# Kernel optimization log

Hardware: AMD Instinct MI355X
Metric: run time of the kernel (lower is better)

## Reference

```python
import jax, jax.numpy as jnp
import numpy as np

B, N, H = 8, 256, 768
P = 128          # path_hidden_size
HEADS = 12
D = H // HEADS   # 64
EPS = 1e-5


def layer_norm(x, g, b):
    mu = jnp.mean(x, axis=-1, keepdims=True)
    var = jnp.mean((x - mu) ** 2, axis=-1, keepdims=True)
    return (x - mu) * jax.lax.rsqrt(var + EPS) * g + b


def setup_inputs() -> dict:
    key = jax.random.key(0)
    ks = jax.random.split(key, 16)
    s = 0.02
    return {
        "nodes": jax.random.normal(ks[0], (B, N, H), jnp.float32),
        "bias": jax.random.normal(ks[1], (B, HEADS, N, N), jnp.float32),
        "paths": jax.random.normal(ks[2], (B, N, N, P), jnp.float32),
        "Wq": jax.random.normal(ks[3], (H, H), jnp.float32) * s,
        "bq": jnp.zeros((H,), jnp.float32),
        "Wk": jax.random.normal(ks[4], (H, H), jnp.float32) * s,
        "bk": jnp.zeros((H,), jnp.float32),
        "Wv": jax.random.normal(ks[5], (H, H), jnp.float32) * s,
        "bv": jnp.zeros((H,), jnp.float32),
        "Wsk": jax.random.normal(ks[6], (P, D), jnp.float32) * s,
        "bsk": jnp.zeros((D,), jnp.float32),
        "Wsv": jax.random.normal(ks[7], (P, D), jnp.float32) * s,
        "bsv": jnp.zeros((D,), jnp.float32),
        "Wo": jax.random.normal(ks[8], (H, H), jnp.float32) * s,
        "bo": jnp.zeros((H,), jnp.float32),
        "g_path": jnp.ones((P,), jnp.float32),
        "b_path": jnp.zeros((P,), jnp.float32),
        "g_out": jnp.ones((H,), jnp.float32),
        "b_out": jnp.zeros((H,), jnp.float32),
    }


def reference(nodes, bias, paths, Wq, bq, Wk, bk, Wv, bv, Wsk, bsk, Wsv, bsv,
              Wo, bo, g_path, b_path, g_out, b_out):
    # q/k/v: [B,N,H] -> [B,heads,N,D]
    def split(x):
        return x.reshape(B, N, HEADS, D).transpose(0, 2, 1, 3)

    q = split(nodes @ Wq + bq)
    k = split(nodes @ Wk + bk)
    v = split(nodes @ Wv + bv)

    pn = layer_norm(paths, g_path, b_path)          # [B,N,N,P]
    struct_k = pn @ Wsk + bsk                       # [B,N,N,D]
    struct_v = pn @ Wsv + bsv                       # [B,N,N,D]

    q = q * (D ** -0.5)
    # content scores + per-query-row structural scores + bias
    w = (jnp.einsum('bhqd,bhkd->bhqk', q, k)
         + jnp.einsum('bhqd,bqkd->bhqk', q, struct_k)
         + bias)
    w = jax.nn.softmax(w, axis=-1)                  # [B,heads,N,N]

    out = (jnp.einsum('bhqk,bhkd->bhqd', w, v)
           + jnp.einsum('bhqk,bqkd->bhqd', w, struct_v))
    out = out.transpose(0, 2, 1, 3).reshape(B, N, H)  # combine heads
    out = jax.nn.relu(out @ Wo + bo)
    # dropout is identity in eval mode
    return layer_norm(nodes + out, g_out, b_out)
```

## Files before the change

### kernel.cpp

```cpp
#include <hip/hip_runtime.h>
#include <stdint.h>

#define Bb 8
#define Nn 256
#define Hh 768
#define Pp 128
#define HEADS 12
#define Dd 64
#define EPSf 1e-5f

typedef __attribute__((ext_vector_type(8))) short bhalf8;
typedef __attribute__((ext_vector_type(4))) float f32x4;

__device__ __forceinline__ unsigned short f2bf(float f) {
    union { float f; unsigned u; } v; v.f = f;
    unsigned r = v.u + 0x7FFFu + ((v.u >> 16) & 1u);
    return (unsigned short)(r >> 16);
}

__global__ __launch_bounds__(256) void k_transpose4(const float* __restrict__ a0, const float* __restrict__ a1,
                                                    const float* __restrict__ a2, const float* __restrict__ a3,
                                                    unsigned short* __restrict__ o0, unsigned short* __restrict__ o1,
                                                    unsigned short* __restrict__ o2, unsigned short* __restrict__ o3) {
    __shared__ float tile[32][33];
    int z = blockIdx.z;
    const float* in = (z == 0) ? a0 : (z == 1) ? a1 : (z == 2) ? a2 : a3;
    unsigned short* out = (z == 0) ? o0 : (z == 1) ? o1 : (z == 2) ? o2 : o3;
    const int R = 768, C = 768;
    int c0 = blockIdx.x * 32, r0 = blockIdx.y * 32;
    int tx = threadIdx.x & 31, ty = threadIdx.x >> 5;
    for (int i = ty; i < 32; i += 8)
        tile[i][tx] = in[(size_t)(r0 + i) * C + c0 + tx];
    __syncthreads();
    for (int i = ty; i < 32; i += 8)
        out[(size_t)(c0 + i) * R + r0 + tx] = f2bf(tile[tx][i]);
}

__global__ __launch_bounds__(256) void k_transpose_small(const float* __restrict__ a0, const float* __restrict__ a1,
                                                         unsigned short* __restrict__ o0, unsigned short* __restrict__ o1) {
    __shared__ float tile[32][33];
    int z = blockIdx.z;
    const float* in = (z == 0) ? a0 : a1;
    unsigned short* out = (z == 0) ? o0 : o1;
    const int R = 128, C = 64;
    int c0 = blockIdx.x * 32, r0 = blockIdx.y * 32;
    int tx = threadIdx.x & 31, ty = threadIdx.x >> 5;
    for (int i = ty; i < 32; i += 8)
        tile[i][tx] = in[(size_t)(r0 + i) * C + c0 + tx];
    __syncthreads();
    for (int i = ty; i < 32; i += 8)
        out[(size_t)(c0 + i) * R + r0 + tx] = f2bf(tile[tx][i]);
}

__global__ __launch_bounds__(256) void k_qkv(const float* __restrict__ nodes,
                                             const unsigned short* __restrict__ Wt,
                                             const float* __restrict__ bq, const float* __restrict__ bk,
                                             const float* __restrict__ bv,
                                             float* __restrict__ qs, float* __restrict__ kk,
                                             float* __restrict__ vv) {
    __shared__ __align__(16) unsigned short Alds[64 * 72];
    __shared__ __align__(16) unsigned short Blds[128 * 72];
    int tid = threadIdx.x;
    int m0 = blockIdx.y * 64;
    int n0 = blockIdx.x * 128;
    int w = tid >> 6, lane = tid & 63;
    int wm = w >> 1, wn = w & 1;
    int lm = lane & 15, lq = lane >> 4;
    f32x4 acc[2][4];
#pragma unroll
    for (int i = 0; i < 2; i++)
#pragma unroll
        for (int j = 0; j < 4; j++) acc[i][j] = (f32x4){0.f, 0.f, 0.f, 0.f};

    for (int kt = 0; kt < 768; kt += 64) {
#pragma unroll
        for (int t = 0; t < 4; t++) {
            int c = t * 256 + tid;
            int row = c >> 4, cc = c & 15;
            float4 v = *(const float4*)(nodes + (size_t)(m0 + row) * 768 + kt + cc * 4);
            uint2 uu;
            uu.x = (unsigned)f2bf(v.x) | ((unsigned)f2bf(v.y) << 16);
            uu.y = (unsigned)f2bf(v.z) | ((unsigned)f2bf(v.w) << 16);
            *(uint2*)(Alds + row * 72 + cc * 4) = uu;
        }
#pragma unroll
        for (int t = 0; t < 4; t++) {
            int c = t * 256 + tid;
            int n = c >> 3, kc = c & 7;
            uint4 v = *(const uint4*)(Wt + (size_t)(n0 + n) * 768 + kt + kc * 8);
            *(uint4*)(Blds + n * 72 + kc * 8) = v;
        }
        __syncthreads();
#pragma unroll
        for (int ks = 0; ks < 2; ks++) {
            bhalf8 af[2];
#pragma unroll
            for (int mi = 0; mi < 2; mi++)
                af[mi] = *(const bhalf8*)(Alds + (wm * 32 + mi * 16 + lm) * 72 + ks * 32 + lq * 8);
#pragma unroll
            for (int nt = 0; nt < 4; nt++) {
                bhalf8 bf = *(const bhalf8*)(Blds + (wn * 64 + nt * 16 + lm) * 72 + ks * 32 + lq * 8);
#pragma unroll
                for (int mi = 0; mi < 2; mi++)
                    acc[mi][nt] = __builtin_amdgcn_mfma_f32_16x16x32_bf16(af[mi], bf, acc[mi][nt], 0, 0, 0);
            }
        }
        __syncthreads();
    }
    int wsel = n0 / 768;
    int nb = n0 % 768;
    const float* bias = (wsel == 0) ? bq : (wsel == 1) ? bk : bv;
    float* dst = (wsel == 0) ? qs : (wsel == 1) ? kk : vv;
    float scale = (wsel == 0) ? 0.125f : 1.0f;
#pragma unroll
    for (int mi = 0; mi < 2; mi++)
#pragma unroll
        for (int nt = 0; nt < 4; nt++)
#pragma unroll
            for (int r = 0; r < 4; r++) {
                int row = m0 + wm * 32 + mi * 16 + lq * 4 + r;
                int col = nb + wn * 64 + nt * 16 + lm;
                int hh = col >> 6, d = col & 63;
                int b = row >> 8, qn = row & 255;
                float val = (acc[mi][nt][r] + bias[col]) * scale;
                dst[(((size_t)b * HEADS + hh) * Nn + qn) * Dd + d] = val;
            }
}

__global__ __launch_bounds__(256) void k_scores(const float* __restrict__ qs,
                                                const float* __restrict__ kk,
                                                const float* __restrict__ bias,
                                                float* __restrict__ wg) {
    __shared__ __align__(16) unsigned short Alds[64 * 72];
    __shared__ __align__(16) unsigned short Blds[64 * 72];
    int tid = threadIdx.x;
    int bh = blockIdx.z;
    int m0 = blockIdx.y * 64;
    int n0 = blockIdx.x * 64;
    int w = tid >> 6, lane = tid & 63, lm = lane & 15, lq = lane >> 4;
    const float* Abase = qs + ((size_t)bh * Nn + m0) * Dd;
    const float* Bbase = kk + ((size_t)bh * Nn + n0) * Dd;
#pragma unroll
    for (int t = 0; t < 4; t++) {
        int c = t * 256 + tid;
        int row = c >> 4, cc = c & 15;
        float4 va = *(const float4*)(Abase + (size_t)row * 64 + cc * 4);
        uint2 ua;
        ua.x = (unsigned)f2bf(va.x) | ((unsigned)f2bf(va.y) << 16);
        ua.y = (unsigned)f2bf(va.z) | ((unsigned)f2bf(va.w) << 16);
        *(uint2*)(Alds + row * 72 + cc * 4) = ua;
        float4 vb = *(const float4*)(Bbase + (size_t)row * 64 + cc * 4);
        uint2 ub;
        ub.x = (unsigned)f2bf(vb.x) | ((unsigned)f2bf(vb.y) << 16);
        ub.y = (unsigned)f2bf(vb.z) | ((unsigned)f2bf(vb.w) << 16);
        *(uint2*)(Blds + row * 72 + cc * 4) = ub;
    }
    __syncthreads();
    f32x4 acc[4];
#pragma unroll
    for (int i = 0; i < 4; i++) acc[i] = (f32x4){0.f, 0.f, 0.f, 0.f};
#pragma unroll
    for (int ks = 0; ks < 2; ks++) {
        bhalf8 af = *(const bhalf8*)(Alds + (w * 16 + lm) * 72 + ks * 32 + lq * 8);
#pragma unroll
        for (int nt = 0; nt < 4; nt++) {
            bhalf8 bf = *(const bhalf8*)(Blds + (nt * 16 + lm) * 72 + ks * 32 + lq * 8);
            acc[nt] = __builtin_amdgcn_mfma_f32_16x16x32_bf16(af, bf, acc[nt], 0, 0, 0);
        }
    }
#pragma unroll
    for (int nt = 0; nt < 4; nt++)
#pragma unroll
        for (int r = 0; r < 4; r++) {
            int row = m0 + w * 16 + lq * 4 + r;
            int col = n0 + nt * 16 + lm;
            size_t idx = ((size_t)bh * Nn + row) * Nn + col;
            wg[idx] = acc[nt][r] + bias[idx];
        }
}

__global__ __launch_bounds__(256) void k_structproj(const float* __restrict__ paths,
                                                    const unsigned short* __restrict__ Wskvt,
                                                    const float* __restrict__ gp, const float* __restrict__ bp,
                                                    const float* __restrict__ bsk, const float* __restrict__ bsv,
                                                    unsigned short* __restrict__ skv) {
    __shared__ __align__(16) unsigned short pn[64 * 136];
    __shared__ __align__(16) unsigned short Bt[128 * 136];
    int tid = threadIdx.x;
    size_t r0 = (size_t)blockIdx.x * 64;
    int w = tid >> 6, lane = tid & 63, lm = lane & 15, lq = lane >> 4;
#pragma unroll
    for (int t = 0; t < 8; t++) {
        int c = t * 256 + tid;
        int n = c >> 4, kc = c & 15;
        uint4 v = *(const uint4*)(Wskvt + n * 128 + kc * 8);
        *(uint4*)(Bt + n * 136 + kc * 8) = v;
    }
    float4 g0 = *(const float4*)(gp + lm * 4);
    float4 g1 = *(const float4*)(gp + 64 + lm * 4);
    float4 bb0 = *(const float4*)(bp + lm * 4);
    float4 bb1 = *(const float4*)(bp + 64 + lm * 4);
#pragma unroll
    for (int it = 0; it < 4; it++) {
        int row_l = w * 16 + it * 4 + lq;
        size_t row = r0 + row_l;
        const float* pr = paths + row * 128;
        float4 x0 = *(const float4*)(pr + lm * 4);
        float4 x1 = *(const float4*)(pr + 64 + lm * 4);
        float s = (x0.x + x0.y) + (x0.z + x0.w) + (x1.x + x1.y) + (x1.z + x1.w);
        float s2 = x0.x * x0.x + x0.y * x0.y + x0.z * x0.z + x0.w * x0.w
                 + x1.x * x1.x + x1.y * x1.y + x1.z * x1.z + x1.w * x1.w;
#pragma unroll
        for (int mk = 1; mk < 16; mk <<= 1) {
            s += __shfl_xor(s, mk);
            s2 += __shfl_xor(s2, mk);
        }
        float mu = s * (1.f / 128.f);
        float var = s2 * (1.f / 128.f) - mu * mu;
        float rs = rsqrtf(var + EPSf);
        float p0 = (x0.x - mu) * rs * g0.x + bb0.x;
        float p1 = (x0.y - mu) * rs * g0.y + bb0.y;
        float p2 = (x0.z - mu) * rs * g0.z + bb0.z;
        float p3 = (x0.w - mu) * rs * g0.w + bb0.w;
        float p4 = (x1.x - mu) * rs * g1.x + bb1.x;
        float p5 = (x1.y - mu) * rs * g1.y + bb1.y;
        float p6 = (x1.z - mu) * rs * g1.z + bb1.z;
        float p7 = (x1.w - mu) * rs * g1.w + bb1.w;
        uint2 ua, ub;
        ua.x = (unsigned)f2bf(p0) | ((unsigned)f2bf(p1) << 16);
        ua.y = (unsigned)f2bf(p2) | ((unsigned)f2bf(p3) << 16);
        ub.x = (unsigned)f2bf(p4) | ((unsigned)f2bf(p5) << 16);
        ub.y = (unsigned)f2bf(p6) | ((unsigned)f2bf(p7) << 16);
        *(uint2*)(pn + row_l * 136 + lm * 4) = ua;
        *(uint2*)(pn + row_l * 136 + 64 + lm * 4) = ub;
    }
    __syncthreads();
    f32x4 acc[8];
#pragma unroll
    for (int i = 0; i < 8; i++) acc[i] = (f32x4){0.f, 0.f, 0.f, 0.f};
#pragma unroll
    for (int ks = 0; ks < 4; ks++) {
        bhalf8 af = *(const bhalf8*)(pn + (w * 16 + lm) * 136 + ks * 32 + lq * 8);
#pragma unroll
        for (int nt = 0; nt < 8; nt++) {
            bhalf8 bf = *(const bhalf8*)(Bt + (nt * 16 + lm) * 136 + ks * 32 + lq * 8);
            acc[nt] = __builtin_amdgcn_mfma_f32_16x16x32_bf16(af, bf, acc[nt], 0, 0, 0);
        }
    }
    __syncthreads();
#pragma unroll
    for (int nt = 0; nt < 8; nt++) {
        int col = nt * 16 + lm;
        float bias = (col < 64) ? bsk[col] : bsv[col - 64];
#pragma unroll
        for (int r = 0; r < 4; r++) {
            int row_l = w * 16 + lq * 4 + r;
            pn[row_l * 136 + col] = f2bf(acc[nt][r] + bias);
        }
    }
    __syncthreads();
#pragma unroll
    for (int i = 0; i < 4; i++) {
        int c = i * 256 + tid;
        int row = c >> 4, chunk = c & 15;
        uint4 v = *(const uint4*)(pn + row * 136 + chunk * 8);
        *(uint4*)(skv + (r0 + row) * 128 + chunk * 8) = v;
    }
}

__global__ __launch_bounds__(256) void k_attn(const float* __restrict__ qs,
                                              const unsigned short* __restrict__ skv,
                                              float* __restrict__ wg,
                                              float* __restrict__ attn) {
    __shared__ __align__(16) unsigned short SKV[256 * 72];
    __shared__ __align__(16) unsigned short A2[16 * 264];
    __shared__ __align__(16) unsigned short Ql[16 * 72];
    __shared__ float redm[16][4];
    __shared__ float reds[16][4];
    int tid = threadIdx.x;
    int bq = blockIdx.x;
    int b = bq >> 8, q = bq & 255;
    int w = tid >> 6, lane = tid & 63, lm = lane & 15, lq = lane >> 4;
    if (tid < 192) {
        int h = tid >> 4, dc = (tid & 15) * 4;
        float4 v = *(const float4*)(qs + (((size_t)b * HEADS + h) * Nn + q) * Dd + dc);
        uint2 u;
        u.x = (unsigned)f2bf(v.x) | ((unsigned)f2bf(v.y) << 16);
        u.y = (unsigned)f2bf(v.z) | ((unsigned)f2bf(v.w) << 16);
        *(uint2*)(Ql + h * 72 + dc) = u;
    } else {
        int t = tid - 192;
        int h = 12 + (t >> 4), dc = (t & 15) * 4;
        uint2 z; z.x = 0; z.y = 0;
        *(uint2*)(Ql + h * 72 + dc) = z;
    }
    const unsigned short* rowb = skv + (size_t)bq * 256 * 128;
#pragma unroll
    for (int i = 0; i < 8; i++) {
        int c = i * 256 + tid;
        int k = c >> 3, j = c & 7;
        uint4 v = *(const uint4*)(rowb + (size_t)k * 128 + j * 8);
        *(uint4*)(SKV + k * 72 + j * 8) = v;
    }
    __syncthreads();
    f32x4 acc1[4];
#pragma unroll
    for (int i = 0; i < 4; i++) acc1[i] = (f32x4){0.f, 0.f, 0.f, 0.f};
#pragma unroll
    for (int ks = 0; ks < 2; ks++) {
        bhalf8 af = *(const bhalf8*)(Ql + lm * 72 + ks * 32 + lq * 8);
#pragma unroll
        for (int nt = 0; nt < 4; nt++) {
            int n0 = (w * 4 + nt) * 16;
            bhalf8 bf = *(const bhalf8*)(SKV + (n0 + lm) * 72 + ks * 32 + lq * 8);
            acc1[nt] = __builtin_amdgcn_mfma_f32_16x16x32_bf16(af, bf, acc1[nt], 0, 0, 0);
        }
    }
    size_t wbase = ((size_t)b * HEADS) * Nn * Nn + (size_t)q * Nn;
    float S[4][4];
#pragma unroll
    for (int nt = 0; nt < 4; nt++)
#pragma unroll
        for (int r = 0; r < 4; r++) {
            int row = lq * 4 + r;
            int col = (w * 4 + nt) * 16 + lm;
            float wgv = (row < 12) ? wg[wbase + (size_t)row * (Nn * Nn) + col] : 0.f;
            S[nt][r] = acc1[nt][r] + wgv;
        }
    float m4[4];
#pragma unroll
    for (int r = 0; r < 4; r++)
        m4[r] = fmaxf(fmaxf(S[0][r], S[1][r]), fmaxf(S[2][r], S[3][r]));
#pragma unroll
    for (int mk = 1; mk < 16; mk <<= 1)
#pragma unroll
        for (int r = 0; r < 4; r++) m4[r] = fmaxf(m4[r], __shfl_xor(m4[r], mk));
    if (lm == 0) {
#pragma unroll
        for (int r = 0; r < 4; r++) redm[lq * 4 + r][w] = m4[r];
    }
    __syncthreads();
    float rowmax[4];
#pragma unroll
    for (int r = 0; r < 4; r++) {
        int row = lq * 4 + r;
        rowmax[r] = fmaxf(fmaxf(redm[row][0], redm[row][1]), fmaxf(redm[row][2], redm[row][3]));
    }
    float P[4][4], psum[4];
#pragma unroll
    for (int r = 0; r < 4; r++) {
#pragma unroll
        for (int nt = 0; nt < 4; nt++) P[nt][r] = __expf(S[nt][r] - rowmax[r]);
        psum[r] = (P[0][r] + P[1][r]) + (P[2][r] + P[3][r]);
    }
#pragma unroll
    for (int mk = 1; mk < 16; mk <<= 1)
#pragma unroll
        for (int r = 0; r < 4; r++) psum[r] += __shfl_xor(psum[r], mk);
    if (lm == 0) {
#pragma unroll
        for (int r = 0; r < 4; r++) reds[lq * 4 + r][w] = psum[r];
    }
    __syncthreads();
    float inv[4];
#pragma unroll
    for (int r = 0; r < 4; r++) {
        int row = lq * 4 + r;
        inv[r] = 1.f / (((reds[row][0] + reds[row][1]) + (reds[row][2] + reds[row][3])));
    }
#pragma unroll
    for (int nt = 0; nt < 4; nt++)
#pragma unroll
        for (int r = 0; r < 4; r++) {
            int row = lq * 4 + r;
            int col = (w * 4 + nt) * 16 + lm;
            float p = P[nt][r] * inv[r];
            A2[row * 264 + col] = f2bf(p);
            if (row < 12) wg[wbase + (size_t)row * (Nn * Nn) + col] = p;
        }
#pragma unroll
    for (int i = 0; i < 8; i++) {
        int c = i * 256 + tid;
        int k = c >> 3, j = c & 7;
        uint4 v = *(const uint4*)(rowb + (size_t)k * 128 + 64 + j * 8);
        *(uint4*)(SKV + k * 72 + j * 8) = v;
    }
    __syncthreads();
    f32x4 acc2 = (f32x4){0.f, 0.f, 0.f, 0.f};
#pragma unroll
    for (int ks = 0; ks < 8; ks++) {
        bhalf8 af = *(const bhalf8*)(A2 + lm * 264 + ks * 32 + lq * 8);
        bhalf8 bf;
#pragma unroll
        for (int j = 0; j < 8; j++)
            bf[j] = (short)SKV[(ks * 32 + lq * 8 + j) * 72 + w * 16 + lm];
        acc2 = __builtin_amdgcn_mfma_f32_16x16x32_bf16(af, bf, acc2, 0, 0, 0);
    }
#pragma unroll
    for (int r = 0; r < 4; r++) {
        int row = lq * 4 + r;
        if (row < 12) attn[(size_t)bq * Hh + row * 64 + w * 16 + lm] = acc2[r];
    }
}

__global__ __launch_bounds__(256) void k_ctxout(const float* __restrict__ wg,
                                                const float* __restrict__ vv,
                                                float* __restrict__ attn) {
    __shared__ __align__(16) float Al[64 * 68];
    __shared__ __align__(16) float Bl[64 * 68];
    int tid = threadIdx.x;
    int bh = blockIdx.y;
    int m0 = blockIdx.x * 64;
    int b = bh / 12, h = bh % 12;
    int tx = tid & 15, ty = tid >> 4;
    int c0 = tx * 4, r0 = ty * 4;
    float acc[4][4];
#pragma unroll
    for (int i = 0; i < 4; i++)
#pragma unroll
        for (int j = 0; j < 4; j++) acc[i][j] = 0.f;
    const float* Abase = wg + ((size_t)bh * Nn + m0) * Nn;
    const float* Bbase = vv + (size_t)bh * Nn * Dd;
    for (int kt = 0; kt < 256; kt += 64) {
#pragma unroll
        for (int t = 0; t < 4; t++) {
            int c = t * 256 + tid;
            int row = c >> 4, cc = c & 15;
            *(float4*)(Al + row * 68 + cc * 4) = *(const float4*)(Abase + (size_t)row * 256 + kt + cc * 4);
            *(float4*)(Bl + row * 68 + cc * 4) = *(const float4*)(Bbase + (size_t)(kt + row) * 64 + cc * 4);
        }
        __syncthreads();
#pragma unroll 8
        for (int k = 0; k < 64; k++) {
            float4 bv4 = *(const float4*)(Bl + k * 68 + c0);
            float a0 = Al[(r0 + 0) * 68 + k];
            float a1 = Al[(r0 + 1) * 68 + k];
            float a2 = Al[(r0 + 2) * 68 + k];
            float a3 = Al[(r0 + 3) * 68 + k];
            acc[0][0] += a0 * bv4.x; acc[0][1] += a0 * bv4.y; acc[0][2] += a0 * bv4.z; acc[0][3] += a0 * bv4.w;
            acc[1][0] += a1 * bv4.x; acc[1][1] += a1 * bv4.y; acc[1][2] += a1 * bv4.z; acc[1][3] += a1 * bv4.w;
            acc[2][0] += a2 * bv4.x; acc[2][1] += a2 * bv4.y; acc[2][2] += a2 * bv4.z; acc[2][3] += a2 * bv4.w;
            acc[3][0] += a3 * bv4.x; acc[3][1] += a3 * bv4.y; acc[3][2] += a3 * bv4.z; acc[3][3] += a3 * bv4.w;
        }
        __syncthreads();
    }
#pragma unroll
    for (int i = 0; i < 4; i++)
#pragma unroll
        for (int j = 0; j < 4; j++) {
            size_t o = ((size_t)b * Nn + m0 + r0 + i) * Hh + h * 64 + c0 + j;
            attn[o] += acc[i][j];
        }
}

__global__ __launch_bounds__(256) void k_outproj(const float* __restrict__ attn,
                                                 const unsigned short* __restrict__ Wot,
                                                 const float* __restrict__ bo,
                                                 const float* __restrict__ nodes,
                                                 float* __restrict__ tmp) {
    __shared__ __align__(16) unsigned short Alds[64 * 72];
    __shared__ __align__(16) unsigned short Blds[128 * 72];
    int tid = threadIdx.x;
    int m0 = blockIdx.y * 64;
    int n0 = blockIdx.x * 128;
    int w = tid >> 6, lane = tid & 63;
    int wm = w >> 1, wn = w & 1;
    int lm = lane & 15, lq = lane >> 4;
    f32x4 acc[2][4];
#pragma unroll
    for (int i = 0; i < 2; i++)
#pragma unroll
        for (int j = 0; j < 4; j++) acc[i][j] = (f32x4){0.f, 0.f, 0.f, 0.f};
    for (int kt = 0; kt < 768; kt += 64) {
#pragma unroll
        for (int t = 0; t < 4; t++) {
            int c = t * 256 + tid;
            int row = c >> 4, cc = c & 15;
            float4 v = *(const float4*)(attn + (size_t)(m0 + row) * 768 + kt + cc * 4);
            uint2 uu;
            uu.x = (unsigned)f2bf(v.x) | ((unsigned)f2bf(v.y) << 16);
            uu.y = (unsigned)f2bf(v.z) | ((unsigned)f2bf(v.w) << 16);
            *(uint2*)(Alds + row * 72 + cc * 4) = uu;
        }
#pragma unroll
        for (int t = 0; t < 4; t++) {
            int c = t * 256 + tid;
            int n = c >> 3, kc = c & 7;
            uint4 v = *(const uint4*)(Wot + (size_t)(n0 + n) * 768 + kt + kc * 8);
            *(uint4*)(Blds + n * 72 + kc * 8) = v;
        }
        __syncthreads();
#pragma unroll
        for (int ks = 0; ks < 2; ks++) {
            bhalf8 af[2];
#pragma unroll
            for (int mi = 0; mi < 2; mi++)
                af[mi] = *(const bhalf8*)(Alds + (wm * 32 + mi * 16 + lm) * 72 + ks * 32 + lq * 8);
#pragma unroll
            for (int nt = 0; nt < 4; nt++) {
                bhalf8 bf = *(const bhalf8*)(Blds + (wn * 64 + nt * 16 + lm) * 72 + ks * 32 + lq * 8);
#pragma unroll
                for (int mi = 0; mi < 2; mi++)
                    acc[mi][nt] = __builtin_amdgcn_mfma_f32_16x16x32_bf16(af[mi], bf, acc[mi][nt], 0, 0, 0);
            }
        }
        __syncthreads();
    }
#pragma unroll
    for (int mi = 0; mi < 2; mi++)
#pragma unroll
        for (int nt = 0; nt < 4; nt++)
#pragma unroll
            for (int r = 0; r < 4; r++) {
                int row = m0 + wm * 32 + mi * 16 + lq * 4 + r;
                int col = n0 + wn * 64 + nt * 16 + lm;
                float val = acc[mi][nt][r] + bo[col];
                val = fmaxf(val, 0.f) + nodes[(size_t)row * 768 + col];
                tmp[(size_t)row * 768 + col] = val;
            }
}

__global__ __launch_bounds__(256) void k_finalln(const float* __restrict__ tmp,
                                                 const float* __restrict__ go,
                                                 const float* __restrict__ bout,
                                                 float* __restrict__ out) {
    __shared__ float rs1[4], rs2[4];
    int m = blockIdx.x, tid = threadIdx.x;
    int lane = tid & 63, wid = tid >> 6;
    const float* row = tmp + (size_t)m * 768;
    float x0 = row[tid], x1 = row[tid + 256], x2 = row[tid + 512];
    float s = x0 + x1 + x2;
    float s2 = x0 * x0 + x1 * x1 + x2 * x2;
#pragma unroll
    for (int mk = 32; mk; mk >>= 1) {
        s += __shfl_xor(s, mk);
        s2 += __shfl_xor(s2, mk);
    }
    if (lane == 0) { rs1[wid] = s; rs2[wid] = s2; }
    __syncthreads();
    s = rs1[0] + rs1[1] + rs1[2] + rs1[3];
    s2 = rs2[0] + rs2[1] + rs2[2] + rs2[3];
    float mu = s * (1.f / 768.f);
    float var = s2 * (1.f / 768.f) - mu * mu;
    float rstd = rsqrtf(var + EPSf);
    float* orow = out + (size_t)m * 768;
    orow[tid] = (x0 - mu) * rstd * go[tid] + bout[tid];
    orow[tid + 256] = (x1 - mu) * rstd * go[tid + 256] + bout[tid + 256];
    orow[tid + 512] = (x2 - mu) * rstd * go[tid + 512] + bout[tid + 512];
}

extern "C" void kernel_launch(void* const* d_in, const int* in_sizes, int n_in,
                              void* d_out, int out_size, void* d_ws, size_t ws_size,
                              hipStream_t stream) {
    const float* nodes = (const float*)d_in[0];
    const float* bias  = (const float*)d_in[1];
    const float* paths = (const float*)d_in[2];
    const float* Wq = (const float*)d_in[3];  const float* bq  = (const float*)d_in[4];
    const float* Wk = (const float*)d_in[5];  const float* bk  = (const float*)d_in[6];
    const float* Wv = (const float*)d_in[7];  const float* bv  = (const float*)d_in[8];
    const float* Wsk = (const float*)d_in[9]; const float* bsk = (const float*)d_in[10];
    const float* Wsv = (const float*)d_in[11];const float* bsv = (const float*)d_in[12];
    const float* Wo = (const float*)d_in[13]; const float* bo  = (const float*)d_in[14];
    const float* gp = (const float*)d_in[15]; const float* bp  = (const float*)d_in[16];
    const float* go = (const float*)d_in[17]; const float* bout= (const float*)d_in[18];
    float* out = (float*)d_out;

    char* ws = (char*)d_ws;
    size_t off = 0;
    auto carve = [&](size_t bytes) -> char* {
        char* p = ws + off;
        off += (bytes + 255) & ~(size_t)255;
        return p;
    };
    float* qs   = (float*)carve((size_t)Bb * HEADS * Nn * Dd * 4);
    float* kk   = (float*)carve((size_t)Bb * HEADS * Nn * Dd * 4);
    float* vv   = (float*)carve((size_t)Bb * HEADS * Nn * Dd * 4);
    float* wg   = (float*)carve((size_t)Bb * HEADS * Nn * Nn * 4);
    float* attn = (float*)carve((size_t)Bb * Nn * Hh * 4);
    float* tmp  = (float*)carve((size_t)Bb * Nn * Hh * 4);
    unsigned short* Wqkvt = (unsigned short*)carve((size_t)3 * 768 * 768 * 2);
    unsigned short* Wot   = (unsigned short*)carve((size_t)768 * 768 * 2);
    unsigned short* Wskvt = (unsigned short*)carve((size_t)128 * 128 * 2);
    unsigned short* skv   = (unsigned short*)carve((size_t)Bb * Nn * Nn * 128 * 2);
    (void)ws_size; (void)in_sizes; (void)n_in; (void)out_size;

    hipLaunchKernelGGL(k_transpose4, dim3(24, 24, 4), dim3(256), 0, stream,
                       Wq, Wk, Wv, Wo,
                       Wqkvt, Wqkvt + (size_t)768 * 768, Wqkvt + (size_t)2 * 768 * 768, Wot);
    hipLaunchKernelGGL(k_transpose_small, dim3(2, 4, 2), dim3(256), 0, stream,
                       Wsk, Wsv, Wskvt, Wskvt + (size_t)64 * 128);

    hipLaunchKernelGGL(k_qkv, dim3(18, 32), dim3(256), 0, stream, nodes, Wqkvt, bq, bk, bv, qs, kk, vv);
    hipLaunchKernelGGL(k_scores, dim3(4, 4, 96), dim3(256), 0, stream, qs, kk, bias, wg);
    hipLaunchKernelGGL(k_structproj, dim3(8192), dim3(256), 0, stream, paths, Wskvt, gp, bp, bsk, bsv, skv);
    hipLaunchKernelGGL(k_attn, dim3(2048), dim3(256), 0, stream, qs, skv, wg, attn);
    hipLaunchKernelGGL(k_ctxout, dim3(4, 96), dim3(256), 0, stream, wg, vv, attn);
    hipLaunchKernelGGL(k_outproj, dim3(6, 32), dim3(256), 0, stream, attn, Wot, bo, nodes, tmp);
    hipLaunchKernelGGL(k_finalln, dim3(2048), dim3(256), 0, stream, tmp, go, bout, out);
}
```

Baseline: 559.5 us.

## Fuse path layernorm and struct projection into attention kernel, fold LN affine into weights

Removes the separate k_structproj kernel and its 268MB bf16 skv intermediate: each attention block now reads its row of paths, layer-normalizes in registers and projects through MFMA directly, keeping struct_k/struct_v in LDS. The LN gain is folded into the transposed weights and the LN bias into a precomputed projection bias. struct_v is stored transposed in LDS so the PV MFMA uses vector loads instead of scalar gathers. In exchange each block does more register-heavy work, with a launch bound asking for two blocks per CU.

```diff
diff --git a/kernel.cpp b/kernel.cpp
--- a/kernel.cpp
+++ b/kernel.cpp
@@ -37,6 +37,7 @@
 }
 
 __global__ __launch_bounds__(256) void k_transpose_small(const float* __restrict__ a0, const float* __restrict__ a1,
+                                                         const float* __restrict__ gp,
                                                          unsigned short* __restrict__ o0, unsigned short* __restrict__ o1) {
     __shared__ float tile[32][33];
     int z = blockIdx.z;
@@ -48,8 +49,21 @@
     for (int i = ty; i < 32; i += 8)
         tile[i][tx] = in[(size_t)(r0 + i) * C + c0 + tx];
     __syncthreads();
+    float g = gp[r0 + tx];
     for (int i = ty; i < 32; i += 8)
-        out[(size_t)(c0 + i) * R + r0 + tx] = f2bf(tile[tx][i]);
+        out[(size_t)(c0 + i) * R + r0 + tx] = f2bf(tile[tx][i] * g);
+}
+
+__global__ __launch_bounds__(128) void k_prep_bias(const float* __restrict__ Wsk, const float* __restrict__ Wsv,
+                                                   const float* __restrict__ bp,
+                                                   const float* __restrict__ bsk, const float* __restrict__ bsv,
+                                                   float* __restrict__ bskv2) {
+    int d = threadIdx.x;
+    const float* W = (d < 64) ? Wsk : Wsv;
+    int dd = d & 63;
+    float s = (d < 64) ? bsk[dd] : bsv[dd];
+    for (int p2 = 0; p2 < 128; p2++) s += bp[p2] * W[p2 * 64 + dd];
+    bskv2[d] = s;
 }
 
 __global__ __launch_bounds__(256) void k_qkv(const float* __restrict__ nodes,
@@ -179,154 +193,157 @@
         }
 }
 
-__global__ __launch_bounds__(256) void k_structproj(const float* __restrict__ paths,
-                                                    const unsigned short* __restrict__ Wskvt,
-                                                    const float* __restrict__ gp, const float* __restrict__ bp,
-                                                    const float* __restrict__ bsk, const float* __restrict__ bsv,
-                                                    unsigned short* __restrict__ skv) {
-    __shared__ __align__(16) unsigned short pn[64 * 136];
-    __shared__ __align__(16) unsigned short Bt[128 * 136];
-    int tid = threadIdx.x;
-    size_t r0 = (size_t)blockIdx.x * 64;
-    int w = tid >> 6, lane = tid & 63, lm = lane & 15, lq = lane >> 4;
-#pragma unroll
-    for (int t = 0; t < 8; t++) {
-        int c = t * 256 + tid;
-        int n = c >> 4, kc = c & 15;
-        uint4 v = *(const uint4*)(Wskvt + n * 128 + kc * 8);
-        *(uint4*)(Bt + n * 136 + kc * 8) = v;
-    }
-    float4 g0 = *(const float4*)(gp + lm * 4);
-    float4 g1 = *(const float4*)(gp + 64 + lm * 4);
-    float4 bb0 = *(const float4*)(bp + lm * 4);
-    float4 bb1 = *(const float4*)(bp + 64 + lm * 4);
-#pragma unroll
-    for (int it = 0; it < 4; it++) {
-        int row_l = w * 16 + it * 4 + lq;
-        size_t row = r0 + row_l;
-        const float* pr = paths + row * 128;
-        float4 x0 = *(const float4*)(pr + lm * 4);
-        float4 x1 = *(const float4*)(pr + 64 + lm * 4);
-        float s = (x0.x + x0.y) + (x0.z + x0.w) + (x1.x + x1.y) + (x1.z + x1.w);
-        float s2 = x0.x * x0.x + x0.y * x0.y + x0.z * x0.z + x0.w * x0.w
-                 + x1.x * x1.x + x1.y * x1.y + x1.z * x1.z + x1.w * x1.w;
-#pragma unroll
-        for (int mk = 1; mk < 16; mk <<= 1) {
-            s += __shfl_xor(s, mk);
-            s2 += __shfl_xor(s2, mk);
-        }
-        float mu = s * (1.f / 128.f);
-        float var = s2 * (1.f / 128.f) - mu * mu;
-        float rs = rsqrtf(var + EPSf);
-        float p0 = (x0.x - mu) * rs * g0.x + bb0.x;
-        float p1 = (x0.y - mu) * rs * g0.y + bb0.y;
-        float p2 = (x0.z - mu) * rs * g0.z + bb0.z;
-        float p3 = (x0.w - mu) * rs * g0.w + bb0.w;
-        float p4 = (x1.x - mu) * rs * g1.x + bb1.x;
-        float p5 = (x1.y - mu) * rs * g1.y + bb1.y;
-        float p6 = (x1.z - mu) * rs * g1.z + bb1.z;
-        float p7 = (x1.w - mu) * rs * g1.w + bb1.w;
-        uint2 ua, ub;
-        ua.x = (unsigned)f2bf(p0) | ((unsigned)f2bf(p1) << 16);
-        ua.y = (unsigned)f2bf(p2) | ((unsigned)f2bf(p3) << 16);
-        ub.x = (unsigned)f2bf(p4) | ((unsigned)f2bf(p5) << 16);
-        ub.y = (unsigned)f2bf(p6) | ((unsigned)f2bf(p7) << 16);
-        *(uint2*)(pn + row_l * 136 + lm * 4) = ua;
-        *(uint2*)(pn + row_l * 136 + 64 + lm * 4) = ub;
-    }
-    __syncthreads();
-    f32x4 acc[8];
-#pragma unroll
-    for (int i = 0; i < 8; i++) acc[i] = (f32x4){0.f, 0.f, 0.f, 0.f};
-#pragma unroll
-    for (int ks = 0; ks < 4; ks++) {
-        bhalf8 af = *(const bhalf8*)(pn + (w * 16 + lm) * 136 + ks * 32 + lq * 8);
-#pragma unroll
-        for (int nt = 0; nt < 8; nt++) {
-            bhalf8 bf = *(const bhalf8*)(Bt + (nt * 16 + lm) * 136 + ks * 32 + lq * 8);
-            acc[nt] = __builtin_amdgcn_mfma_f32_16x16x32_bf16(af, bf, acc[nt], 0, 0, 0);
-        }
-    }
-    __syncthreads();
-#pragma unroll
-    for (int nt = 0; nt < 8; nt++) {
-        int col = nt * 16 + lm;
-        float bias = (col < 64) ? bsk[col] : bsv[col - 64];
-#pragma unroll
-        for (int r = 0; r < 4; r++) {
-            int row_l = w * 16 + lq * 4 + r;
-            pn[row_l * 136 + col] = f2bf(acc[nt][r] + bias);
-        }
-    }
-    __syncthreads();
-#pragma unroll
-    for (int i = 0; i < 4; i++) {
-        int c = i * 256 + tid;
-        int row = c >> 4, chunk = c & 15;
-        uint4 v = *(const uint4*)(pn + row * 136 + chunk * 8);
-        *(uint4*)(skv + (r0 + row) * 128 + chunk * 8) = v;
-    }
-}
-
-__global__ __launch_bounds__(256) void k_attn(const float* __restrict__ qs,
-                                              const unsigned short* __restrict__ skv,
-                                              float* __restrict__ wg,
-                                              float* __restrict__ attn) {
-    __shared__ __align__(16) unsigned short SKV[256 * 72];
+__global__ __launch_bounds__(256, 2) void k_attn(const float* __restrict__ qs,
+                                                 const float* __restrict__ paths,
+                                                 const unsigned short* __restrict__ Wskvt,
+                                                 const float* __restrict__ bskv2,
+                                                 float* __restrict__ wg,
+                                                 float* __restrict__ attn) {
+    __shared__ __align__(16) unsigned short SKbuf[256 * 72];
     __shared__ __align__(16) unsigned short A2[16 * 264];
-    __shared__ __align__(16) unsigned short Ql[16 * 72];
-    __shared__ float redm[16][4];
-    __shared__ float reds[16][4];
+    __shared__ float redm[64];
+    __shared__ float reds[64];
+    unsigned short* SVT = SKbuf;
+
     int tid = threadIdx.x;
     int bq = blockIdx.x;
     int b = bq >> 8, q = bq & 255;
     int w = tid >> 6, lane = tid & 63, lm = lane & 15, lq = lane >> 4;
-    if (tid < 192) {
-        int h = tid >> 4, dc = (tid & 15) * 4;
-        float4 v = *(const float4*)(qs + (((size_t)b * HEADS + h) * Nn + q) * Dd + dc);
-        uint2 u;
-        u.x = (unsigned)f2bf(v.x) | ((unsigned)f2bf(v.y) << 16);
-        u.y = (unsigned)f2bf(v.z) | ((unsigned)f2bf(v.w) << 16);
-        *(uint2*)(Ql + h * 72 + dc) = u;
-    } else {
-        int t = tid - 192;
-        int h = 12 + (t >> 4), dc = (t & 15) * 4;
-        uint2 z; z.x = 0; z.y = 0;
-        *(uint2*)(Ql + h * 72 + dc) = z;
-    }
-    const unsigned short* rowb = skv + (size_t)bq * 256 * 128;
-#pragma unroll
-    for (int i = 0; i < 8; i++) {
-        int c = i * 256 + tid;
-        int k = c >> 3, j = c & 7;
-        uint4 v = *(const uint4*)(rowb + (size_t)k * 128 + j * 8);
-        *(uint4*)(SKV + k * 72 + j * 8) = v;
-    }
-    __syncthreads();
-    f32x4 acc1[4];
-#pragma unroll
-    for (int i = 0; i < 4; i++) acc1[i] = (f32x4){0.f, 0.f, 0.f, 0.f};
-#pragma unroll
-    for (int ks = 0; ks < 2; ks++) {
-        bhalf8 af = *(const bhalf8*)(Ql + lm * 72 + ks * 32 + lq * 8);
-#pragma unroll
-        for (int nt = 0; nt < 4; nt++) {
-            int n0 = (w * 4 + nt) * 16;
-            bhalf8 bf = *(const bhalf8*)(SKV + (n0 + lm) * 72 + ks * 32 + lq * 8);
-            acc1[nt] = __builtin_amdgcn_mfma_f32_16x16x32_bf16(af, bf, acc1[nt], 0, 0, 0);
-        }
-    }
-    size_t wbase = ((size_t)b * HEADS) * Nn * Nn + (size_t)q * Nn;
-    float S[4][4];
-#pragma unroll
-    for (int nt = 0; nt < 4; nt++)
+
+    bhalf8 af1[2];
+    {
+        bhalf8 z = (bhalf8){0, 0, 0, 0, 0, 0, 0, 0};
+        af1[0] = z; af1[1] = z;
+        if (lm < 12) {
+            const float* qp = qs + (((size_t)b * HEADS + lm) * Nn + q) * Dd;
+#pragma unroll
+            for (int ks = 0; ks < 2; ks++) {
+                float4 v0 = *(const float4*)(qp + ks * 32 + lq * 8);
+                float4 v1 = *(const float4*)(qp + ks * 32 + lq * 8 + 4);
+                bhalf8 t;
+                t[0] = (short)f2bf(v0.x); t[1] = (short)f2bf(v0.y);
+                t[2] = (short)f2bf(v0.z); t[3] = (short)f2bf(v0.w);
+                t[4] = (short)f2bf(v1.x); t[5] = (short)f2bf(v1.y);
+                t[6] = (short)f2bf(v1.z); t[7] = (short)f2bf(v1.w);
+                af1[ks] = t;
+            }
+        }
+    }
+    float bv_[8];
+#pragma unroll
+    for (int nt = 0; nt < 8; nt++) bv_[nt] = bskv2[nt * 16 + lm];
+
+    const float* ppath = paths + (size_t)bq * (256 * 128);
+    f32x4 accSV[2][2][4];
+
+#pragma unroll
+    for (int p = 0; p < 2; p++) {
+        f32x4 acc[2][8];
+#pragma unroll
+        for (int i = 0; i < 2; i++)
+#pragma unroll
+            for (int j = 0; j < 8; j++) acc[i][j] = (f32x4){0.f, 0.f, 0.f, 0.f};
+        bhalf8 afr[2][4];
+#pragma unroll
+        for (int mi = 0; mi < 2; mi++) {
+            int R = w * 64 + p * 32 + mi * 16 + lm;
+            const float* pr = ppath + (size_t)R * 128;
+            float x[32];
+#pragma unroll
+            for (int ks = 0; ks < 4; ks++) {
+                float4 a = *(const float4*)(pr + ks * 32 + lq * 8);
+                float4 c = *(const float4*)(pr + ks * 32 + lq * 8 + 4);
+                x[ks * 8 + 0] = a.x; x[ks * 8 + 1] = a.y; x[ks * 8 + 2] = a.z; x[ks * 8 + 3] = a.w;
+                x[ks * 8 + 4] = c.x; x[ks * 8 + 5] = c.y; x[ks * 8 + 6] = c.z; x[ks * 8 + 7] = c.w;
+            }
+            float s = 0.f, s2 = 0.f;
+#pragma unroll
+            for (int i = 0; i < 32; i++) { s += x[i]; s2 += x[i] * x[i]; }
+            s  += __shfl_xor(s, 16);  s2 += __shfl_xor(s2, 16);
+            s  += __shfl_xor(s, 32);  s2 += __shfl_xor(s2, 32);
+            float mu = s * (1.f / 128.f);
+            float var = s2 * (1.f / 128.f) - mu * mu;
+            float rs = rsqrtf(var + EPSf);
+#pragma unroll
+            for (int ks = 0; ks < 4; ks++) {
+                bhalf8 t;
+#pragma unroll
+                for (int j = 0; j < 8; j++)
+                    t[j] = (short)f2bf((x[ks * 8 + j] - mu) * rs);
+                afr[mi][ks] = t;
+            }
+        }
+#pragma unroll
+        for (int ks = 0; ks < 4; ks++) {
+#pragma unroll
+            for (int nt = 0; nt < 8; nt++) {
+                bhalf8 bf = *(const bhalf8*)(Wskvt + (size_t)(nt * 16 + lm) * 128 + ks * 32 + lq * 8);
+#pragma unroll
+                for (int mi = 0; mi < 2; mi++)
+                    acc[mi][nt] = __builtin_amdgcn_mfma_f32_16x16x32_bf16(afr[mi][ks], bf, acc[mi][nt], 0, 0, 0);
+            }
+        }
+#pragma unroll
+        for (int mi = 0; mi < 2; mi++) {
+#pragma unroll
+            for (int nt = 0; nt < 4; nt++) {
+                int col = nt * 16 + lm;
+#pragma unroll
+                for (int rr = 0; rr < 4; rr++) {
+                    int R2 = w * 64 + p * 32 + mi * 16 + lq * 4 + rr;
+                    SKbuf[R2 * 72 + col] = f2bf(acc[mi][nt][rr] + bv_[nt]);
+                }
+            }
+#pragma unroll
+            for (int nt = 0; nt < 4; nt++) accSV[p][mi][nt] = acc[mi][nt + 4];
+        }
+    }
+    __syncthreads();
+
+    size_t wbase = ((size_t)b * HEADS) * (Nn * Nn) + (size_t)q * Nn;
+    float wgv[4][4];
+#pragma unroll
+    for (int nt = 0; nt < 4; nt++) {
+        int col = w * 64 + nt * 16 + lm;
 #pragma unroll
         for (int r = 0; r < 4; r++) {
             int row = lq * 4 + r;
-            int col = (w * 4 + nt) * 16 + lm;
-            float wgv = (row < 12) ? wg[wbase + (size_t)row * (Nn * Nn) + col] : 0.f;
-            S[nt][r] = acc1[nt][r] + wgv;
-        }
+            wgv[nt][r] = (row < 12) ? wg[wbase + (size_t)row * (Nn * Nn) + col] : 0.f;
+        }
+    }
+    f32x4 acc1[4];
+#pragma unroll
+    for (int i = 0; i < 4; i++) acc1[i] = (f32x4){0.f, 0.f, 0.f, 0.f};
+#pragma unroll
+    for (int ks = 0; ks < 2; ks++) {
+#pragma unroll
+        for (int nt = 0; nt < 4; nt++) {
+            int n0 = w * 64 + nt * 16;
+            bhalf8 bf = *(const bhalf8*)(SKbuf + (n0 + lm) * 72 + ks * 32 + lq * 8);
+            acc1[nt] = __builtin_amdgcn_mfma_f32_16x16x32_bf16(af1[ks], bf, acc1[nt], 0, 0, 0);
+        }
+    }
+    float S[4][4];
+#pragma unroll
+    for (int nt = 0; nt < 4; nt++)
+#pragma unroll
+        for (int r = 0; r < 4; r++) S[nt][r] = acc1[nt][r] + wgv[nt][r];
+
+    __syncthreads();
+#pragma unroll
+    for (int p = 0; p < 2; p++)
+#pragma unroll
+        for (int mi = 0; mi < 2; mi++)
+#pragma unroll
+            for (int nt = 0; nt < 4; nt++) {
+                int d = nt * 16 + lm;
+#pragma unroll
+                for (int rr = 0; rr < 4; rr++) {
+                    int R2 = w * 64 + p * 32 + mi * 16 + lq * 4 + rr;
+                    SVT[d * 264 + R2] = f2bf(accSV[p][mi][nt][rr] + bv_[nt + 4]);
+                }
+            }
+
     float m4[4];
 #pragma unroll
     for (int r = 0; r < 4; r++)
@@ -337,14 +354,15 @@
         for (int r = 0; r < 4; r++) m4[r] = fmaxf(m4[r], __shfl_xor(m4[r], mk));
     if (lm == 0) {
 #pragma unroll
-        for (int r = 0; r < 4; r++) redm[lq * 4 + r][w] = m4[r];
+        for (int r = 0; r < 4; r++) redm[(lq * 4 + r) * 4 + w] = m4[r];
     }
     __syncthreads();
     float rowmax[4];
 #pragma unroll
     for (int r = 0; r < 4; r++) {
         int row = lq * 4 + r;
-        rowmax[r] = fmaxf(fmaxf(redm[row][0], redm[row][1]), fmaxf(redm[row][2], redm[row][3]));
+        rowmax[r] = fmaxf(fmaxf(redm[row * 4 + 0], redm[row * 4 + 1]),
+                          fmaxf(redm[row * 4 + 2], redm[row * 4 + 3]));
     }
     float P[4][4], psum[4];
 #pragma unroll
@@ -359,41 +377,32 @@
         for (int r = 0; r < 4; r++) psum[r] += __shfl_xor(psum[r], mk);
     if (lm == 0) {
 #pragma unroll
-        for (int r = 0; r < 4; r++) reds[lq * 4 + r][w] = psum[r];
+        for (int r = 0; r < 4; r++) reds[(lq * 4 + r) * 4 + w] = psum[r];
     }
     __syncthreads();
     float inv[4];
 #pragma unroll
     for (int r = 0; r < 4; r++) {
         int row = lq * 4 + r;
-        inv[r] = 1.f / (((reds[row][0] + reds[row][1]) + (reds[row][2] + reds[row][3])));
+        inv[r] = 1.f / (((reds[row * 4 + 0] + reds[row * 4 + 1]) + (reds[row * 4 + 2] + reds[row * 4 + 3])));
     }
 #pragma unroll
     for (int nt = 0; nt < 4; nt++)
 #pragma unroll
         for (int r = 0; r < 4; r++) {
             int row = lq * 4 + r;
-            int col = (w * 4 + nt) * 16 + lm;
-            float p = P[nt][r] * inv[r];
-            A2[row * 264 + col] = f2bf(p);
-            if (row < 12) wg[wbase + (size_t)row * (Nn * Nn) + col] = p;
-        }
-#pragma unroll
-    for (int i = 0; i < 8; i++) {
-        int c = i * 256 + tid;
-        int k = c >> 3, j = c & 7;
-        uint4 v = *(const uint4*)(rowb + (size_t)k * 128 + 64 + j * 8);
-        *(uint4*)(SKV + k * 72 + j * 8) = v;
-    }
-    __syncthreads();
+            int col = w * 64 + nt * 16 + lm;
+            float pv = P[nt][r] * inv[r];
+            A2[row * 264 + col] = f2bf(pv);
+            if (row < 12) wg[wbase + (size_t)row * (Nn * Nn) + col] = pv;
+        }
+    __syncthreads();
+
     f32x4 acc2 = (f32x4){0.f, 0.f, 0.f, 0.f};
 #pragma unroll
     for (int ks = 0; ks < 8; ks++) {
         bhalf8 af = *(const bhalf8*)(A2 + lm * 264 + ks * 32 + lq * 8);
-        bhalf8 bf;
-#pragma unroll
-        for (int j = 0; j < 8; j++)
-            bf[j] = (short)SKV[(ks * 32 + lq * 8 + j) * 72 + w * 16 + lm];
+        bhalf8 bf = *(const bhalf8*)(SVT + (w * 16 + lm) * 264 + ks * 32 + lq * 8);
         acc2 = __builtin_amdgcn_mfma_f32_16x16x32_bf16(af, bf, acc2, 0, 0, 0);
     }
 #pragma unroll
@@ -581,19 +590,20 @@
     unsigned short* Wqkvt = (unsigned short*)carve((size_t)3 * 768 * 768 * 2);
     unsigned short* Wot   = (unsigned short*)carve((size_t)768 * 768 * 2);
     unsigned short* Wskvt = (unsigned short*)carve((size_t)128 * 128 * 2);
-    unsigned short* skv   = (unsigned short*)carve((size_t)Bb * Nn * Nn * 128 * 2);
+    float* bskv2 = (float*)carve(128 * 4);
     (void)ws_size; (void)in_sizes; (void)n_in; (void)out_size;
 
     hipLaunchKernelGGL(k_transpose4, dim3(24, 24, 4), dim3(256), 0, stream,
                        Wq, Wk, Wv, Wo,
                        Wqkvt, Wqkvt + (size_t)768 * 768, Wqkvt + (size_t)2 * 768 * 768, Wot);
     hipLaunchKernelGGL(k_transpose_small, dim3(2, 4, 2), dim3(256), 0, stream,
-                       Wsk, Wsv, Wskvt, Wskvt + (size_t)64 * 128);
+                       Wsk, Wsv, gp, Wskvt, Wskvt + (size_t)64 * 128);
+    hipLaunchKernelGGL(k_prep_bias, dim3(1), dim3(128), 0, stream,
+                       Wsk, Wsv, bp, bsk, bsv, bskv2);
 
     hipLaunchKernelGGL(k_qkv, dim3(18, 32), dim3(256), 0, stream, nodes, Wqkvt, bq, bk, bv, qs, kk, vv);
     hipLaunchKernelGGL(k_scores, dim3(4, 4, 96), dim3(256), 0, stream, qs, kk, bias, wg);
-    hipLaunchKernelGGL(k_structproj, dim3(8192), dim3(256), 0, stream, paths, Wskvt, gp, bp, bsk, bsv, skv);
-    hipLaunchKernelGGL(k_attn, dim3(2048), dim3(256), 0, stream, qs, skv, wg, attn);
+    hipLaunchKernelGGL(k_attn, dim3(2048), dim3(256), 0, stream, qs, paths, Wskvt, bskv2, wg, attn);
     hipLaunchKernelGGL(k_ctxout, dim3(4, 96), dim3(256), 0, stream, wg, vv, attn);
     hipLaunchKernelGGL(k_outproj, dim3(6, 32), dim3(256), 0, stream, attn, Wot, bo, nodes, tmp);
     hipLaunchKernelGGL(k_finalln, dim3(2048), dim3(256), 0, stream, tmp, go, bout, out);
```

Measured after the change: 562.1 us. No clear change (+0.5%).
